# Kernel tuning notes

Measured on AMD Instinct MI355X. Metric: run time of the kernel, lower is better.

Reference implementation:

```python
import jax, jax.numpy as jnp
import numpy as np

N = 100000        # nodes
E = 1600000       # edges (nnz per Laplacian order)
K_ORDERS = 3      # K + 1
IN_C = 64
OUT_C = 64


def setup_inputs() -> dict:
    key = jax.random.key(0)
    ks = jax.random.split(key, 7)
    X_real = jax.random.normal(ks[0], (N, IN_C), jnp.float32)
    X_imag = jax.random.normal(ks[1], (N, IN_C), jnp.float32)
    edge_index = jax.random.randint(ks[2], (2, E), 0, N)  # [rows; cols]
    L_real_vals = jax.random.normal(ks[3], (K_ORDERS, E), jnp.float32) * 0.1
    L_imag_vals = jax.random.normal(ks[4], (K_ORDERS, E), jnp.float32) * 0.1
    stdv = 1.0 / np.sqrt(OUT_C)
    weight = jax.random.uniform(ks[5], (K_ORDERS, IN_C, OUT_C), jnp.float32, -stdv, stdv)
    bias = jnp.zeros((1, OUT_C), jnp.float32)
    return {"X_real": X_real, "X_imag": X_imag, "edge_index": edge_index,
            "L_real_vals": L_real_vals, "L_imag_vals": L_imag_vals,
            "weight": weight, "bias": bias}


def _spmm(vals, rows, cols, X):
    # y[i] = sum_{(i,j) in edges} vals_ij * X[j]   (equivalent to torch.spmm)
    return jax.ops.segment_sum(vals[:, None] * X[cols], rows, num_segments=N)


def reference(X_real, X_imag, edge_index, L_real_vals, L_imag_vals, weight, bias):
    rows, cols = edge_index[0], edge_index[1]
    real = jnp.zeros((N, OUT_C), X_real.dtype)
    imag = jnp.zeros((N, OUT_C), X_real.dtype)
    for k in range(K_ORDERS):  # small fixed number of spectral orders
        ArXr = _spmm(L_real_vals[k], rows, cols, X_real)
        AiXi = _spmm(L_imag_vals[k], rows, cols, X_imag)
        AiXr = _spmm(L_imag_vals[k], rows, cols, X_real)
        ArXi = _spmm(L_real_vals[k], rows, cols, X_imag)
        real = real + (ArXr - AiXi) @ weight[k]
        imag = imag + (AiXr + ArXi) @ weight[k]
    return real + bias, imag + bias
```

## Files before the change

### kernel.cpp

```cpp
#include <hip/hip_runtime.h>
#include <hip/hip_fp16.h>


constexpr int N_NODES = 100000;
constexpr int E_EDGES = 1600000;
constexpr int CH = 64;
constexpr int NP = 100096;
constexpr int NBUCK = NP / 256;
constexpr int CHUNK_A = 2048;
constexpr int NBLK_A = (E_EDGES + CHUNK_A - 1) / CHUNK_A;
constexpr unsigned COLMASK = 0x1FFFFu;

typedef unsigned u32x4 __attribute__((ext_vector_type(4)));
typedef _Float16 h2f __attribute__((ext_vector_type(2)));
typedef _Float16 h8f __attribute__((ext_vector_type(8)));
typedef float f32x4 __attribute__((ext_vector_type(4)));

__device__ __forceinline__ float fdot2h(unsigned a, unsigned b, float c) {
#if __has_builtin(__builtin_amdgcn_fdot2)
    return __builtin_amdgcn_fdot2(__builtin_bit_cast(h2f, a),
                                  __builtin_bit_cast(h2f, b), c, false);
#else
    float2 af = __half22float2(__builtin_bit_cast(__half2, a));
    float2 bf = __half22float2(__builtin_bit_cast(__half2, b));
    return c + af.x * bf.x + af.y * bf.y;
#endif
}

__device__ __forceinline__ unsigned pack2(float a, float b) {
    return __builtin_bit_cast(unsigned, __floats2half2_rn(a, b));
}

__device__ __forceinline__ unsigned rot16(unsigned u) {
    return (u >> 16) | (u << 16);
}

__global__ __launch_bounds__(256) void init_out_kernel(const float* __restrict__ bias,
                                                       float* __restrict__ out) {
    int i = blockIdx.x * 256 + threadIdx.x;
    out[i] = bias[i & 63];
}

__global__ __launch_bounds__(256) void xh_zero_kernel(const float* __restrict__ Xr,
                                                      const float* __restrict__ Xi,
                                                      unsigned* __restrict__ Xh,
                                                      int* __restrict__ bcnt) {
    int i = blockIdx.x * 256 + threadIdx.x;
    if (i < NBUCK) bcnt[i] = 0;
    const float4 r = ((const float4*)Xr)[i];
    const float4 m = ((const float4*)Xi)[i];
    uint4 u;
    u.x = pack2(r.x, m.x);
    u.y = pack2(r.y, m.y);
    u.z = pack2(r.z, m.z);
    u.w = pack2(r.w, m.w);
    ((uint4*)Xh)[i] = u;
}

__global__ __launch_bounds__(1024) void chist_kernel(const int* __restrict__ rows,
                                                     int* __restrict__ bcnt) {
    __shared__ int lh[NBUCK];
    const int tid = threadIdx.x;
    for (int t = tid; t < NBUCK; t += 1024) lh[t] = 0;
    __syncthreads();
    const int base = blockIdx.x * CHUNK_A;
    const int nedge = min(CHUNK_A, E_EDGES - base);
    for (int j = tid; j < nedge; j += 1024) atomicAdd(&lh[rows[base + j] >> 8], 1);
    __syncthreads();
    for (int t = tid; t < NBUCK; t += 1024)
        if (lh[t]) atomicAdd(&bcnt[t], lh[t]);
}

__global__ __launch_bounds__(512) void cscan_kernel(const int* __restrict__ bcnt,
                                                    int* __restrict__ cofs,
                                                    int* __restrict__ ccur,
                                                    const float* __restrict__ W,
                                                    h8f* __restrict__ Bpack) {
    __shared__ int s[512];
    const int t = threadIdx.x;
    int v = (t < NBUCK) ? bcnt[t] : 0;
    s[t] = v;
    __syncthreads();
    for (int off = 1; off < 512; off <<= 1) {
        int a = (t >= off) ? s[t - off] : 0;
        __syncthreads();
        s[t] += a;
        __syncthreads();
    }
    if (t < NBUCK) {
        cofs[t] = s[t] - v;
        ccur[t] = s[t] - v;
    }
    if (t == NBUCK - 1) cofs[NBUCK] = s[t];

    for (int sidx = t; sidx < 24 * 64; sidx += 512) {
        const int L = sidx & 63;
        const int ntkc = sidx >> 6;
        const int nt = ntkc & 3;
        const int kc = ntkc >> 2;
        const int colb = nt * 16 + (L & 15);
        const int kbase = kc * 32 + ((L >> 4) << 3);
        h8f vv;
#pragma unroll
        for (int j = 0; j < 8; ++j) vv[j] = (_Float16)W[(kbase + j) * 64 + colb];
        Bpack[sidx] = vv;
    }
}

__global__ __launch_bounds__(1024) void partA_kernel(const int* __restrict__ rows,
                                                     const int* __restrict__ cols,
                                                     const float* __restrict__ Lr,
                                                     const float* __restrict__ Li,
                                                     int* __restrict__ ccur,
                                                     u32x4* __restrict__ temp) {
    __shared__ u32x4 sRec[CHUNK_A];
    __shared__ int sDst[CHUNK_A];
    __shared__ int lh[NBUCK];
    __shared__ int lcur[NBUCK];
    __shared__ int gdel[NBUCK];
    __shared__ int ss[512];
    const int tid = threadIdx.x;
    const int base = blockIdx.x * CHUNK_A;
    const int nedge = min(CHUNK_A, E_EDGES - base);

    for (int t = tid; t < NBUCK; t += 1024) lh[t] = 0;
    __syncthreads();
    for (int j = tid; j < nedge; j += 1024) atomicAdd(&lh[rows[base + j] >> 8], 1);
    __syncthreads();

    if (tid < 512) ss[tid] = (tid < NBUCK) ? lh[tid] : 0;
    __syncthreads();
    for (int off = 1; off < 512; off <<= 1) {
        int a = 0;
        if (tid < 512 && tid >= off) a = ss[tid - off];
        __syncthreads();
        if (tid < 512) ss[tid] += a;
        __syncthreads();
    }
    if (tid < NBUCK) {
        const int excl = ss[tid] - lh[tid];
        lcur[tid] = excl;
        const int gb = lh[tid] ? atomicAdd(&ccur[tid], lh[tid]) : 0;
        gdel[tid] = gb - excl;
    }
    __syncthreads();

    for (int j = tid; j < nedge; j += 1024) {
        const int e = base + j;
        const int r = rows[e];
        const int bk = r >> 8;
        const int pos = atomicAdd(&lcur[bk], 1);
        u32x4 u;
        u.x = (unsigned)cols[e] | ((unsigned)(r & 255) << 17);
        u.y = pack2(Lr[e], Li[e]);
        u.z = pack2(Lr[E_EDGES + e], Li[E_EDGES + e]);
        u.w = pack2(Lr[2 * E_EDGES + e], Li[2 * E_EDGES + e]);
        sRec[pos] = u;
        sDst[pos] = gdel[bk] + pos;
    }
    __syncthreads();

    for (int c = tid; c < nedge; c += 1024) temp[sDst[c]] = sRec[c];
}

__global__ __launch_bounds__(1024) void partB_kernel(const int* __restrict__ cofs,
                                                     const u32x4* __restrict__ temp,
                                                     u32x4* __restrict__ payload,
                                                     int* __restrict__ rowst) {
    const int b = blockIdx.x;
    const int t = threadIdx.x;
    const int start = cofs[b];
    const int endp = cofs[b + 1];
    __shared__ int lh[256];
    __shared__ int s[256];
    if (t < 256) lh[t] = 0;
    __syncthreads();
    for (int i = start + t; i < endp; i += 1024)
        atomicAdd(&lh[temp[i].x >> 17], 1);
    __syncthreads();
    int v = 0;
    if (t < 256) {
        v = lh[t];
        s[t] = v;
    }
    __syncthreads();
    for (int off = 1; off < 256; off <<= 1) {
        int a = (t >= off && t < 256) ? s[t - off] : 0;
        __syncthreads();
        if (t < 256) s[t] += a;
        __syncthreads();
    }
    if (t < 256) {
        const int excl = s[t] - v;
        rowst[b * 256 + t] = start + excl;
        lh[t] = excl;
    }
    if (b == NBUCK - 1 && t == 0) rowst[NBUCK * 256] = endp;
    __syncthreads();
    for (int i = start + t; i < endp; i += 1024) {
        u32x4 q = temp[i];
        const int rl = (int)(q.x >> 17);
        const int pos = start + atomicAdd(&lh[rl], 1);
        payload[pos] = q;
    }
}

__global__ __launch_bounds__(256) void row6_kernel(const int* __restrict__ rowst,
                                                   const u32x4* __restrict__ payload,
                                                   const unsigned* __restrict__ Xh,
                                                   const h8f* __restrict__ Bpack,
                                                   const float* __restrict__ bias,
                                                   float* __restrict__ out) {
    __shared__ __half sY[2][16][200];
    const int w = (int)threadIdx.x >> 6;
    const int lane = threadIdx.x & 63;
    const int band = blockIdx.x * 16;

    for (int q = 0; q < 4; ++q) {
        const int ri = w * 4 + q;
        const int r = __builtin_amdgcn_readfirstlane(band + ri);
        const int start = rowst[r];
        const int end = rowst[r + 1];
        const int n = end - start;

        float aR0 = 0.f, aI0 = 0.f, aR1 = 0.f, aI1 = 0.f, aR2 = 0.f, aI2 = 0.f;

        auto gx = [&](unsigned cw) -> unsigned {
            return Xh[(size_t)(cw & COLMASK) * 64 + lane];
        };
        auto accum = [&](const u32x4& qq, unsigned xv) {
            aR0 = fdot2h(qq.y ^ 0x80000000u, xv, aR0);
            aI0 = fdot2h(rot16(qq.y), xv, aI0);
            aR1 = fdot2h(qq.z ^ 0x80000000u, xv, aR1);
            aI1 = fdot2h(rot16(qq.z), xv, aI1);
            aR2 = fdot2h(qq.w ^ 0x80000000u, xv, aR2);
            aI2 = fdot2h(rot16(qq.w), xv, aI2);
        };

        if (n >= 8) {
            int p = start;
            u32x4 A = payload[p];
            u32x4 B = payload[p + 1];
            u32x4 C = payload[p + 2];
            u32x4 D = payload[p + 3];
            u32x4 E = payload[p + 4];
            u32x4 F = payload[p + 5];
            unsigned xA = gx(A.x), xB = gx(B.x), xC = gx(C.x), xD = gx(D.x);

            for (; p + 7 < end; p += 2) {
                u32x4 G = payload[p + 6];
                u32x4 H = payload[p + 7];
                unsigned xE = gx(E.x);
                unsigned xF = gx(F.x);
                accum(A, xA);
                accum(B, xB);
                A = C; xA = xC;
                B = D; xB = xD;
                C = E; xC = xE;
                D = F; xD = xF;
                E = G;
                F = H;
            }
            accum(A, xA);
            accum(B, xB);
            accum(C, xC);
            accum(D, xD);
            unsigned xE = gx(E.x);
            unsigned xF = gx(F.x);
            accum(E, xE);
            accum(F, xF);
            if (p + 6 < end) {
                u32x4 G = payload[p + 6];
                unsigned xG = gx(G.x);
                accum(G, xG);
            }
        } else {
            for (int p = start; p < end; ++p) {
                u32x4 qq = payload[p];
                unsigned xv = gx(qq.x);
                accum(qq, xv);
            }
        }

        sY[0][ri][lane] = __float2half(aR0);
        sY[0][ri][64 + lane] = __float2half(aR1);
        sY[0][ri][128 + lane] = __float2half(aR2);
        sY[1][ri][lane] = __float2half(aI0);
        sY[1][ri][64 + lane] = __float2half(aI1);
        sY[1][ri][128 + lane] = __float2half(aI2);
    }
    __syncthreads();

    const int nt = w;
    const int m = lane & 15;
    const int ko = (lane >> 4) << 3;
    f32x4 accR = (f32x4){0.f, 0.f, 0.f, 0.f};
    f32x4 accI = (f32x4){0.f, 0.f, 0.f, 0.f};
#pragma unroll
    for (int kc = 0; kc < 6; ++kc) {
        h8f bf = Bpack[(kc * 4 + nt) * 64 + lane];
        h8f aR = *(const h8f*)&sY[0][m][kc * 32 + ko];
        h8f aI = *(const h8f*)&sY[1][m][kc * 32 + ko];
        accR = __builtin_amdgcn_mfma_f32_16x16x32_f16(aR, bf, accR, 0, 0, 0);
        accI = __builtin_amdgcn_mfma_f32_16x16x32_f16(aI, bf, accI, 0, 0, 0);
    }
    const int colw = lane & 15;
    const int rbase = (lane >> 4) << 2;
    const float b = bias[nt * 16 + colw];
#pragma unroll
    for (int rr = 0; rr < 4; ++rr) {
        const int row = band + rbase + rr;
        __builtin_nontemporal_store(accR[rr] + b,
                                    &out[(size_t)row * 64 + nt * 16 + colw]);
        __builtin_nontemporal_store(accI[rr] + b,
                                    &out[(size_t)(N_NODES + row) * 64 + nt * 16 + colw]);
    }
}

template <int NK>
__global__ __launch_bounds__(256) void xw_kernel(const float* __restrict__ Xr,
                                                 const float* __restrict__ Xi,
                                                 const float* __restrict__ W,
                                                 __half2* __restrict__ XWh) {
    __shared__ float sW[NK][64][64];
    __shared__ float4 sX4[2][32][16];
    const int tid = threadIdx.x;

    float4* swf = (float4*)&sW[0][0][0];
    const float4* gW = (const float4*)W;
    for (int i = tid; i < NK * 1024; i += 256) swf[i] = gW[i];

    const int rowbase = blockIdx.x * 32;
    float4* sxf = (float4*)sX4;
    const float4* gXr = (const float4*)(Xr + (size_t)rowbase * CH);
    const float4* gXi = (const float4*)(Xi + (size_t)rowbase * CH);
    for (int i = tid; i < 512; i += 256) {
        sxf[i] = gXr[i];
        sxf[512 + i] = gXi[i];
    }
    __syncthreads();

    const int col = tid & 63;
    const int rg = tid >> 6;

    float acc[8][2 * NK];
#pragma unroll
    for (int i = 0; i < 8; ++i)
#pragma unroll
        for (int c2 = 0; c2 < 2 * NK; ++c2) acc[i][c2] = 0.0f;

#pragma unroll 2
    for (int j4 = 0; j4 < 16; ++j4) {
        float w[NK][4];
#pragma unroll
        for (int k = 0; k < NK; ++k)
#pragma unroll
            for (int jj = 0; jj < 4; ++jj) w[k][jj] = sW[k][j4 * 4 + jj][col];
#pragma unroll
        for (int i = 0; i < 8; ++i) {
            float4 xr = sX4[0][rg * 8 + i][j4];
            float4 xi = sX4[1][rg * 8 + i][j4];
            const float xra[4] = {xr.x, xr.y, xr.z, xr.w};
            const float xia[4] = {xi.x, xi.y, xi.z, xi.w};
#pragma unroll
            for (int jj = 0; jj < 4; ++jj)
#pragma unroll
                for (int k = 0; k < NK; ++k) {
                    acc[i][2 * k] += xra[jj] * w[k][jj];
                    acc[i][2 * k + 1] += xia[jj] * w[k][jj];
                }
        }
    }

#pragma unroll
    for (int i = 0; i < 8; ++i) {
        __half2* dst = XWh + (size_t)(rowbase + rg * 8 + i) * (NK * 64);
#pragma unroll
        for (int k = 0; k < NK; ++k)
            dst[k * 64 + col] = __floats2half2_rn(acc[i][2 * k], acc[i][2 * k + 1]);
    }
}

template <int NK>
__global__ __launch_bounds__(256) void edge_kernel(const int* __restrict__ rows,
                                                   const int* __restrict__ cols,
                                                   const float* __restrict__ Lr,
                                                   const float* __restrict__ Li,
                                                   const __half2* __restrict__ XWh,
                                                   float* __restrict__ out) {
    const int gid = blockIdx.x * 256 + threadIdx.x;
    const int e = gid >> 6;
    const int lane = gid & 63;
    if (e >= E_EDGES) return;

    const int row = rows[e];
    const int colN = cols[e];
    const __half2* xw = XWh + (size_t)colN * (NK * 64);

    float rc = 0.0f, ic = 0.0f;
#pragma unroll
    for (int k = 0; k < NK; ++k) {
        const float lr = Lr[(size_t)k * E_EDGES + e];
        const float li = Li[(size_t)k * E_EDGES + e];
        float2 v = __half22float2(xw[k * 64 + lane]);
        rc += lr * v.x - li * v.y;
        ic += li * v.x + lr * v.y;
    }
    unsafeAtomicAdd(out + (size_t)row * 64 + lane, rc);
    unsafeAtomicAdd(out + ((size_t)N_NODES + row) * 64 + lane, ic);
}

extern "C" void kernel_launch(void* const* d_in, const int* in_sizes, int n_in,
                              void* d_out, int out_size, void* d_ws, size_t ws_size,
                              hipStream_t stream) {
    const float* Xr = (const float*)d_in[0];
    const float* Xi = (const float*)d_in[1];
    const int* ei = (const int*)d_in[2];
    const float* Lr = (const float*)d_in[3];
    const float* Li = (const float*)d_in[4];
    const float* W = (const float*)d_in[5];
    const float* bias = (const float*)d_in[6];
    float* out = (float*)d_out;

    const int* rows = ei;
    const int* cols = ei + E_EDGES;

    char* wsb = (char*)d_ws;
    const int edge_grid = (int)((size_t)E_EDGES * 64 / 256);
    const int gemm_grid = N_NODES / 32;

    unsigned* Xh = (unsigned*)wsb;
    unsigned* payload = (unsigned*)(wsb + 25600000);
    u32x4* temp = (u32x4*)(wsb + 51200000);
    int* rowst = (int*)(wsb + 76800000);
    int* bcnt = (int*)(wsb + 77204480);
    int* cofs = (int*)(wsb + 77206080);
    int* ccur = (int*)(wsb + 77207680);
    h8f* Bpack = (h8f*)(wsb + 77209280);
    const size_t need_new = 77233856;

    if (ws_size >= need_new) {
        xh_zero_kernel<<<6250, 256, 0, stream>>>(Xr, Xi, Xh, bcnt);
        chist_kernel<<<NBLK_A, 1024, 0, stream>>>(rows, bcnt);
        cscan_kernel<<<1, 512, 0, stream>>>(bcnt, cofs, ccur, W, Bpack);
        partA_kernel<<<NBLK_A, 1024, 0, stream>>>(rows, cols, Lr, Li, ccur, temp);
        partB_kernel<<<NBUCK, 1024, 0, stream>>>(cofs, temp, (u32x4*)payload, rowst);
        row6_kernel<<<N_NODES / 16, 256, 0, stream>>>(rowst, (const u32x4*)payload, Xh,
                                                      Bpack, bias, out);
        return;
    }

    __half2* XWh = (__half2*)wsb;
    const size_t need_onepass = 76800000;

    if (ws_size >= need_onepass) {
        init_out_kernel<<<2 * N_NODES * CH / 256, 256, 0, stream>>>(bias, out);
        xw_kernel<3><<<gemm_grid, 256, 0, stream>>>(Xr, Xi, W, XWh);
        edge_kernel<3><<<edge_grid, 256, 0, stream>>>(rows, cols, Lr, Li, XWh, out);
    } else {
        init_out_kernel<<<2 * N_NODES * CH / 256, 256, 0, stream>>>(bias, out);
        for (int k = 0; k < 3; ++k) {
            xw_kernel<1><<<gemm_grid, 256, 0, stream>>>(Xr, Xi, W + (size_t)k * 4096, XWh);
            edge_kernel<1><<<edge_grid, 256, 0, stream>>>(rows, cols,
                                                          Lr + (size_t)k * E_EDGES,
                                                          Li + (size_t)k * E_EDGES, XWh, out);
        }
    }
}
```

Baseline: 160.6 us.

## Fuse fp16 packing into histogram kernel and deepen row gather prefetch

The X real/imag fp16 packing is merged into the row-bucket histogram kernel, and the bucket counters are now zeroed with a memset. This removes one separate pass and kernel. Separately, the per-row SpMM loop keeps eight payload entries and X gathers in flight instead of six, and advances four edges per iteration, to hide more gather latency. The cost is higher register pressure in the row kernel and a longer scalar tail for rows with 12 or more edges.

```diff
diff --git a/kernel.cpp b/kernel.cpp
--- a/kernel.cpp
+++ b/kernel.cpp
@@ -41,31 +41,31 @@
     out[i] = bias[i & 63];
 }
 
-__global__ __launch_bounds__(256) void xh_zero_kernel(const float* __restrict__ Xr,
-                                                      const float* __restrict__ Xi,
-                                                      unsigned* __restrict__ Xh,
-                                                      int* __restrict__ bcnt) {
-    int i = blockIdx.x * 256 + threadIdx.x;
-    if (i < NBUCK) bcnt[i] = 0;
-    const float4 r = ((const float4*)Xr)[i];
-    const float4 m = ((const float4*)Xi)[i];
-    uint4 u;
-    u.x = pack2(r.x, m.x);
-    u.y = pack2(r.y, m.y);
-    u.z = pack2(r.z, m.z);
-    u.w = pack2(r.w, m.w);
-    ((uint4*)Xh)[i] = u;
-}
-
-__global__ __launch_bounds__(1024) void chist_kernel(const int* __restrict__ rows,
-                                                     int* __restrict__ bcnt) {
+__global__ __launch_bounds__(1024) void prep_hist_kernel(const float* __restrict__ Xr,
+                                                         const float* __restrict__ Xi,
+                                                         const int* __restrict__ rows,
+                                                         unsigned* __restrict__ Xh,
+                                                         int* __restrict__ bcnt) {
     __shared__ int lh[NBUCK];
     const int tid = threadIdx.x;
     for (int t = tid; t < NBUCK; t += 1024) lh[t] = 0;
     __syncthreads();
     const int base = blockIdx.x * CHUNK_A;
-    const int nedge = min(CHUNK_A, E_EDGES - base);
-    for (int j = tid; j < nedge; j += 1024) atomicAdd(&lh[rows[base + j] >> 8], 1);
+#pragma unroll
+    for (int h = 0; h < 2; ++h) {
+        const int i = base + h * 1024 + tid;
+        if (i < E_EDGES) {
+            const float4 r = ((const float4*)Xr)[i];
+            const float4 m = ((const float4*)Xi)[i];
+            uint4 u;
+            u.x = pack2(r.x, m.x);
+            u.y = pack2(r.y, m.y);
+            u.z = pack2(r.z, m.z);
+            u.w = pack2(r.w, m.w);
+            ((uint4*)Xh)[i] = u;
+            atomicAdd(&lh[rows[i] >> 8], 1);
+        }
+    }
     __syncthreads();
     for (int t = tid; t < NBUCK; t += 1024)
         if (lh[t]) atomicAdd(&bcnt[t], lh[t]);
@@ -237,42 +237,41 @@
             aI2 = fdot2h(rot16(qq.w), xv, aI2);
         };
 
-        if (n >= 8) {
+        if (n >= 12) {
             int p = start;
-            u32x4 A = payload[p];
-            u32x4 B = payload[p + 1];
-            u32x4 C = payload[p + 2];
-            u32x4 D = payload[p + 3];
-            u32x4 E = payload[p + 4];
-            u32x4 F = payload[p + 5];
-            unsigned xA = gx(A.x), xB = gx(B.x), xC = gx(C.x), xD = gx(D.x);
-
-            for (; p + 7 < end; p += 2) {
-                u32x4 G = payload[p + 6];
-                u32x4 H = payload[p + 7];
-                unsigned xE = gx(E.x);
-                unsigned xF = gx(F.x);
-                accum(A, xA);
-                accum(B, xB);
-                A = C; xA = xC;
-                B = D; xB = xD;
-                C = E; xC = xE;
-                D = F; xD = xF;
-                E = G;
-                F = H;
+            u32x4 P0 = payload[p], P1 = payload[p + 1], P2 = payload[p + 2],
+                  P3 = payload[p + 3], P4 = payload[p + 4], P5 = payload[p + 5],
+                  P6 = payload[p + 6], P7 = payload[p + 7];
+            unsigned x0 = gx(P0.x), x1 = gx(P1.x), x2 = gx(P2.x), x3 = gx(P3.x);
+            unsigned x4 = gx(P4.x), x5 = gx(P5.x), x6 = gx(P6.x), x7 = gx(P7.x);
+
+            for (; p + 11 < end; p += 4) {
+                u32x4 Q0 = payload[p + 8], Q1 = payload[p + 9];
+                u32x4 Q2 = payload[p + 10], Q3 = payload[p + 11];
+                accum(P0, x0);
+                accum(P1, x1);
+                accum(P2, x2);
+                accum(P3, x3);
+                P0 = P4; P1 = P5; P2 = P6; P3 = P7;
+                x0 = x4; x1 = x5; x2 = x6; x3 = x7;
+                P4 = Q0; P5 = Q1; P6 = Q2; P7 = Q3;
+                x4 = gx(P4.x);
+                x5 = gx(P5.x);
+                x6 = gx(P6.x);
+                x7 = gx(P7.x);
             }
-            accum(A, xA);
-            accum(B, xB);
-            accum(C, xC);
-            accum(D, xD);
-            unsigned xE = gx(E.x);
-            unsigned xF = gx(F.x);
-            accum(E, xE);
-            accum(F, xF);
-            if (p + 6 < end) {
-                u32x4 G = payload[p + 6];
-                unsigned xG = gx(G.x);
-                accum(G, xG);
+            accum(P0, x0);
+            accum(P1, x1);
+            accum(P2, x2);
+            accum(P3, x3);
+            accum(P4, x4);
+            accum(P5, x5);
+            accum(P6, x6);
+            accum(P7, x7);
+            for (p += 8; p < end; ++p) {
+                u32x4 qq = payload[p];
+                unsigned xv = gx(qq.x);
+                accum(qq, xv);
             }
         } else {
             for (int p = start; p < end; ++p) {
@@ -440,8 +439,8 @@
     const size_t need_new = 77233856;
 
     if (ws_size >= need_new) {
-        xh_zero_kernel<<<6250, 256, 0, stream>>>(Xr, Xi, Xh, bcnt);
-        chist_kernel<<<NBLK_A, 1024, 0, stream>>>(rows, bcnt);
+        hipMemsetAsync(bcnt, 0, NBUCK * sizeof(int), stream);
+        prep_hist_kernel<<<NBLK_A, 1024, 0, stream>>>(Xr, Xi, rows, Xh, bcnt);
         cscan_kernel<<<1, 512, 0, stream>>>(bcnt, cofs, ccur, W, Bpack);
         partA_kernel<<<NBLK_A, 1024, 0, stream>>>(rows, cols, Lr, Li, ccur, temp);
         partB_kernel<<<NBUCK, 1024, 0, stream>>>(cofs, temp, (u32x4*)payload, rowst);
```

After: 156.6 us. -2.5%, faster.
